# Kernel tuning notes

Measured on AMD Instinct MI355X. Metric: run time of the kernel, lower is better.

Reference implementation:

```python
import jax, jax.numpy as jnp
import numpy as np

N = 100000   # num nodes
E = 500000   # num hyperedges
NNZ = 1600000
H, C = 4, 32
IN_CH = 128


def setup_inputs() -> dict:
    key = jax.random.key(0)
    k1, k2, k3, k4, k5 = jax.random.split(key, 5)
    X = jax.random.normal(k1, (N, IN_CH), dtype=jnp.float32)
    W = jax.random.normal(k2, (IN_CH, H * C), dtype=jnp.float32) * (1.0 / np.sqrt(IN_CH))
    att_e = jax.random.normal(k3, (1, H, C), dtype=jnp.float32) * 0.1
    vertex = jax.random.randint(k4, (NNZ,), 0, N, dtype=jnp.int64)
    edges = jax.random.randint(k5, (NNZ,), 0, E, dtype=jnp.int64)
    return {"X": X, "W": W, "att_e": att_e, "vertex": vertex, "edges": edges}


def reference(X, W, att_e, vertex, edges):
    n = X.shape[0]
    X0 = X @ W                                  # [N, H*C]
    Xh = X0.reshape(n, H, C)                    # [N, H, C]
    Xve = Xh[vertex]                            # [nnz, H, C] gather
    # scatter-mean over hyperedges
    esum = jax.ops.segment_sum(Xve, edges, num_segments=E)            # [E, H, C]
    cnt = jax.ops.segment_sum(jnp.ones((Xve.shape[0],), X.dtype), edges, num_segments=E)
    Xe = esum / jnp.maximum(cnt, 1.0)[:, None, None]                  # [E, H, C]
    # per-edge attention score
    alpha_e = (Xe * att_e).sum(-1)              # [E, H]
    a_ev = alpha_e[edges]                       # [nnz, H]
    alpha = jax.nn.leaky_relu(a_ev, 0.01)
    # segment softmax over vertex groups
    m = jax.ops.segment_max(alpha, vertex, num_segments=n)            # [N, H]
    ex = jnp.exp(alpha - m[vertex])
    den = jax.ops.segment_sum(ex, vertex, num_segments=n)             # [N, H]
    alpha = ex / (den[vertex] + 1e-16)          # [nnz, H]
    # weighted scatter-sum back to nodes
    Xev = Xe[edges] * alpha[:, :, None]         # [nnz, H, C]
    Xv = jax.ops.segment_sum(Xev, vertex, num_segments=n)             # [N, H, C]
    return Xv.reshape(n, H * C) + X0
```

## Files before the change

### kernel.cpp

```cpp
#include <hip/hip_runtime.h>
#include <hip/hip_bf16.h>
#include <hip/hip_fp16.h>
#include <cstdint>

#define NH 4
#define HC 128
#define INCH 128
#define NEDGE 500000
#define NN 100000

#define KE_SHIFT 11
#define KV_SHIFT 9
#define KE (1 << KE_SHIFT)
#define KV (1 << KV_SHIFT)
#define NBE 245
#define NBV 196
#define CAP_E 8192
#define CAP_V 10240
#define CHUNK_A 8192
#define NB_ABS 64

typedef float          f32x2 __attribute__((ext_vector_type(2)));
typedef float          f32x4 __attribute__((ext_vector_type(4)));
typedef float          f32x8 __attribute__((ext_vector_type(8)));
typedef unsigned int   u32x2 __attribute__((ext_vector_type(2)));
typedef unsigned int   u32x4 __attribute__((ext_vector_type(4)));
typedef unsigned short u16x8 __attribute__((ext_vector_type(8)));

static __device__ __forceinline__ unsigned short f2bf(float f){
  union { float f; unsigned u; } v; v.f = f;
  unsigned r = v.u + 0x7fffu + ((v.u >> 16) & 1u);
  return (unsigned short)(r >> 16);
}
static __device__ __forceinline__ float bf2f(unsigned short b){
  union { unsigned u; float f; } v; v.u = ((unsigned)b) << 16;
  return v.f;
}
static __device__ __forceinline__ f32x8 bf8f(u16x8 b){
  f32x8 r;
  r[0]=bf2f(b[0]); r[1]=bf2f(b[1]); r[2]=bf2f(b[2]); r[3]=bf2f(b[3]);
  r[4]=bf2f(b[4]); r[5]=bf2f(b[5]); r[6]=bf2f(b[6]); r[7]=bf2f(b[7]);
  return r;
}

#if __has_builtin(__builtin_amdgcn_cvt_pk_fp8_f32) && __has_builtin(__builtin_amdgcn_cvt_pk_f32_fp8)
#define FP8_HW 1
#else
#define FP8_HW 0
#endif

#if !FP8_HW
static __device__ __forceinline__ unsigned enc1_fp8(float v){
  union{ __half h; unsigned short u; } c; c.h = __float2half(v);
  unsigned u = c.u;
  unsigned s = (u>>15)&1u, e=(u>>10)&31u, m=u&0x3FFu;
  int e8 = (int)e - 8;
  unsigned lsb = (m>>7)&1u;
  unsigned m8 = (m + 63u + lsb) >> 7;
  if (m8 == 8u){ m8 = 0u; e8 += 1; }
  if (e8 <= 0)  return s<<7;
  if (e8 >= 16) return (s<<7)|0x7Eu;
  return (s<<7)|((unsigned)e8<<3)|m8;
}
static __device__ __forceinline__ float dec1_fp8(unsigned b){
  unsigned s=(b>>7)&1u, e=(b>>3)&15u, m=b&7u;
  union{unsigned u; float f;} r;
  if (e==0u){ r.f = (float)m * 0.001953125f; if(s) r.f = -r.f; }
  else r.u = (s<<31)|((e+120u)<<23)|(m<<20);
  return r.f;
}
#endif

static __device__ __forceinline__ u32x2 pack8_fp8(const f32x8 v){
  u32x2 w;
#if FP8_HW
  int w0 = __builtin_amdgcn_cvt_pk_fp8_f32(v[0], v[1], 0, false);
  w0     = __builtin_amdgcn_cvt_pk_fp8_f32(v[2], v[3], w0, true);
  int w1 = __builtin_amdgcn_cvt_pk_fp8_f32(v[4], v[5], 0, false);
  w1     = __builtin_amdgcn_cvt_pk_fp8_f32(v[6], v[7], w1, true);
  w.x = (unsigned)w0; w.y = (unsigned)w1;
#else
  w.x = enc1_fp8(v[0]) | (enc1_fp8(v[1])<<8) | (enc1_fp8(v[2])<<16) | (enc1_fp8(v[3])<<24);
  w.y = enc1_fp8(v[4]) | (enc1_fp8(v[5])<<8) | (enc1_fp8(v[6])<<16) | (enc1_fp8(v[7])<<24);
#endif
  return w;
}
static __device__ __forceinline__ void fma8_fp8(f32x8& acc, float c, u32x2 q){
#if FP8_HW
  f32x2 p;
  p = __builtin_amdgcn_cvt_pk_f32_fp8((int)q.x, false); acc[0] += c*p.x; acc[1] += c*p.y;
  p = __builtin_amdgcn_cvt_pk_f32_fp8((int)q.x, true ); acc[2] += c*p.x; acc[3] += c*p.y;
  p = __builtin_amdgcn_cvt_pk_f32_fp8((int)q.y, false); acc[4] += c*p.x; acc[5] += c*p.y;
  p = __builtin_amdgcn_cvt_pk_f32_fp8((int)q.y, true ); acc[6] += c*p.x; acc[7] += c*p.y;
#else
  acc[0] += c*dec1_fp8(q.x&0xFF);        acc[1] += c*dec1_fp8((q.x>>8)&0xFF);
  acc[2] += c*dec1_fp8((q.x>>16)&0xFF);  acc[3] += c*dec1_fp8(q.x>>24);
  acc[4] += c*dec1_fp8(q.y&0xFF);        acc[5] += c*dec1_fp8((q.y>>8)&0xFF);
  acc[6] += c*dec1_fp8((q.y>>16)&0xFF);  acc[7] += c*dec1_fp8(q.y>>24);
#endif
}

#define GBM 128
#define GBK 16
__global__ __launch_bounds__(256, 2) void gemm_x0(const float* __restrict__ X,
                                                  const float* __restrict__ Wm,
                                                  unsigned short* __restrict__ X0bf, int nrows){
  __shared__ float As[GBK][GBM+4];
  __shared__ float Bs[GBK][HC+4];
  const int tid  = threadIdx.x;
  const int row0 = blockIdx.x * GBM;
  const int trow = tid >> 4;
  const int tcol = tid & 15;
  float acc[8][8];
  #pragma unroll
  for (int i=0;i<8;i++)
    #pragma unroll
    for (int j=0;j<8;j++) acc[i][j]=0.f;

  for (int k0=0;k0<INCH;k0+=GBK){
    #pragma unroll
    for (int l = tid; l < 512; l += 256){
      int r  = l >> 2;
      int ks = (l & 3) * 4;
      int grow = row0 + r;
      float4 v = make_float4(0.f,0.f,0.f,0.f);
      if (grow < nrows) v = *(const float4*)(X + (size_t)grow*INCH + k0 + ks);
      As[ks+0][r]=v.x; As[ks+1][r]=v.y; As[ks+2][r]=v.z; As[ks+3][r]=v.w;
    }
    #pragma unroll
    for (int l = tid; l < 512; l += 256){
      int r  = l >> 5;
      int cs = (l & 31) * 4;
      float4 v = *(const float4*)(Wm + (size_t)(k0+r)*HC + cs);
      *(float4*)(&Bs[r][cs]) = v;
    }
    __syncthreads();
    #pragma unroll
    for (int kk=0;kk<GBK;kk++){
      float a[8], b[8];
      *(float4*)&a[0] = *(float4*)&As[kk][trow*8];
      *(float4*)&a[4] = *(float4*)&As[kk][trow*8+4];
      *(float4*)&b[0] = *(float4*)&Bs[kk][tcol*8];
      *(float4*)&b[4] = *(float4*)&Bs[kk][tcol*8+4];
      #pragma unroll
      for (int i=0;i<8;i++)
        #pragma unroll
        for (int j=0;j<8;j++) acc[i][j] = fmaf(a[i], b[j], acc[i][j]);
    }
    __syncthreads();
  }
  #pragma unroll
  for (int i=0;i<8;i++){
    int grow = row0 + trow*8 + i;
    if (grow < nrows){
      ushort4 b0, b1;
      b0.x=f2bf(acc[i][0]); b0.y=f2bf(acc[i][1]); b0.z=f2bf(acc[i][2]); b0.w=f2bf(acc[i][3]);
      b1.x=f2bf(acc[i][4]); b1.y=f2bf(acc[i][5]); b1.z=f2bf(acc[i][6]); b1.w=f2bf(acc[i][7]);
      *(ushort4*)(X0bf + (size_t)grow*HC + tcol*8    ) = b0;
      *(ushort4*)(X0bf + (size_t)grow*HC + tcol*8 + 4) = b1;
    }
  }
}

__global__ __launch_bounds__(512) void phaseA(const unsigned short* __restrict__ X0bf,
                                              unsigned* __restrict__ gmaxU, int n8,
                                              const int* __restrict__ vertex,
                                              const int* __restrict__ edges, int nnz,
                                              int* __restrict__ cursE, int* __restrict__ cursV,
                                              unsigned* __restrict__ stgE, unsigned* __restrict__ stgV){
  __shared__ int cE[NBE], c2E[NBE], gE[NBE];
  __shared__ int cV[NBV], c2V[NBV], gV[NBV];
  __shared__ float red[8];
  const int t = threadIdx.x;

  if ((int)blockIdx.x < NB_ABS){
    float pm = 0.f;
    for (int i = blockIdx.x*512 + t; i < n8; i += NB_ABS*512){
      u16x8 v = *(const u16x8*)(X0bf + (size_t)i*8);
      f32x8 f = bf8f(v);
      #pragma unroll
      for (int j=0;j<8;j++) pm = fmaxf(pm, fabsf(f[j]));
    }
    #pragma unroll
    for (int s=1; s<64; s<<=1) pm = fmaxf(pm, __shfl_xor(pm, s, 64));
    const int wid = t >> 6;
    if ((t & 63) == 0) red[wid] = pm;
    __syncthreads();
    if (t == 0){
      float m = red[0];
      #pragma unroll
      for (int j=1;j<8;j++) m = fmaxf(m, red[j]);
      atomicMax(gmaxU, __float_as_uint(m));
    }
    return;
  }

  const int base = (blockIdx.x - NB_ABS) * CHUNK_A;
  int ev[16], vv[16];
  #pragma unroll
  for (int j=0;j<16;j++){
    int i = base + t + j*512;
    if (i < nnz){ ev[j] = edges[i]; vv[j] = vertex[i]; }
    else ev[j] = -1;
  }
  for (int j=t;j<NBE;j+=512){ cE[j]=0; c2E[j]=0; }
  for (int j=t;j<NBV;j+=512){ cV[j]=0; c2V[j]=0; }
  __syncthreads();
  #pragma unroll
  for (int j=0;j<16;j++) if (ev[j]>=0){
    atomicAdd(&cE[ev[j]>>KE_SHIFT], 1);
    atomicAdd(&cV[vv[j]>>KV_SHIFT], 1);
  }
  __syncthreads();
  for (int j=t;j<NBE;j+=512) gE[j] = atomicAdd(&cursE[j], cE[j]);
  for (int j=t;j<NBV;j+=512) gV[j] = atomicAdd(&cursV[j], cV[j]);
  __syncthreads();
  #pragma unroll
  for (int j=0;j<16;j++) if (ev[j]>=0){
    int bE = ev[j]>>KE_SHIFT;
    int p = gE[bE] + atomicAdd(&c2E[bE],1);
    if (p < CAP_E) stgE[(size_t)bE*CAP_E + p] = ((unsigned)vv[j] << KE_SHIFT) | (unsigned)(ev[j] & (KE-1));
    int bV = vv[j]>>KV_SHIFT;
    int q = gV[bV] + atomicAdd(&c2V[bV],1);
    if (q < CAP_V) stgV[(size_t)bV*CAP_V + q] = ((unsigned)ev[j] << KV_SHIFT) | (unsigned)(vv[j] & (KV-1));
  }
}

template<int K, int CAP, int IT, int SHIFT, int NB>
__device__ __forceinline__ void phaseB_body(const unsigned* __restrict__ stg,
                                            const int* __restrict__ curs,
                                            int* __restrict__ offsOut,
                                            int* __restrict__ csrOut, int nKeys, int b,
                                            int* cur, int* tsum, int* bsh){
  const int t = threadIdx.x;
  const int k0 = b * K;
  const int kc = min(K, nKeys - k0);
  int c = (t < NB) ? min(curs[t], CAP) : 0;
  bsh[t] = c; __syncthreads();
  for (int d2=1; d2<512; d2<<=1){
    int x = (t>=d2) ? bsh[t-d2] : 0; __syncthreads();
    bsh[t] += x; __syncthreads();
  }
  const int gbase = (b > 0) ? bsh[b-1] : 0;
  const int cnt   = min(curs[b], CAP);
  if (b == NB-1 && t == 0) offsOut[nKeys] = bsh[NB-1];
  unsigned it[IT];
  #pragma unroll
  for (int j=0;j<IT;j++){
    int i = t + j*512;
    it[j] = (i < cnt) ? stg[(size_t)b*CAP + i] : 0xFFFFFFFFu;
  }
  for (int j=t;j<K;j+=512) cur[j] = 0;
  __syncthreads();
  #pragma unroll
  for (int j=0;j<IT;j++) if (it[j] != 0xFFFFFFFFu) atomicAdd(&cur[it[j] & (K-1)], 1);
  __syncthreads();
  constexpr int KPT = K / 512;
  int loc[KPT]; int s = 0;
  #pragma unroll
  for (int j=0;j<KPT;j++){ loc[j] = s; s += cur[t*KPT + j]; }
  tsum[t] = s; __syncthreads();
  for (int d2=1; d2<512; d2<<=1){
    int x = (t>=d2) ? tsum[t-d2] : 0; __syncthreads();
    tsum[t] += x; __syncthreads();
  }
  const int tbase = tsum[t] - s;
  __syncthreads();
  #pragma unroll
  for (int j=0;j<KPT;j++){
    int k = t*KPT + j;
    int abs0 = gbase + tbase + loc[j];
    if (k < kc) offsOut[k0 + k] = abs0;
    cur[k] = abs0;
  }
  __syncthreads();
  #pragma unroll
  for (int j=0;j<IT;j++) if (it[j] != 0xFFFFFFFFu){
    int pos = atomicAdd(&cur[it[j] & (K-1)], 1);
    csrOut[pos] = (int)(it[j] >> SHIFT);
  }
}

__global__ __launch_bounds__(512) void phaseB_fused(const unsigned* __restrict__ stgE,
                                                    const unsigned* __restrict__ stgV,
                                                    const int* __restrict__ cursE,
                                                    const int* __restrict__ cursV,
                                                    int* __restrict__ eoffs, int* __restrict__ voffs,
                                                    int* __restrict__ ecsr, int* __restrict__ vcsr){
  __shared__ int cur[KE];
  __shared__ int tsum[512];
  __shared__ int bsh[512];
  const int b = blockIdx.x;
  if (b < NBE) phaseB_body<KE, CAP_E, CAP_E/512, KE_SHIFT, NBE>(stgE, cursE, eoffs, ecsr, NEDGE, b, cur, tsum, bsh);
  else         phaseB_body<KV, CAP_V, CAP_V/512, KV_SHIFT, NBV>(stgV, cursV, voffs, vcsr, NN, b - NBE, cur, tsum, bsh);
}

__global__ __launch_bounds__(256) void edge_agg(const unsigned short* __restrict__ X0bf,
                                                const float* __restrict__ att,
                                                const int* __restrict__ ecsr,
                                                const int* __restrict__ eoffs,
                                                const unsigned* __restrict__ gmaxU,
                                                unsigned char* __restrict__ Xe8,
                                                unsigned* __restrict__ alphaS, int E){
  int eg = blockIdx.x * 16 + (threadIdx.x >> 4);
  if (eg >= E) return;
  const int lane  = threadIdx.x & 15;
  const unsigned cbase = lane * 8;
  const float qs = 448.0f / fmaxf(__uint_as_float(*gmaxU), 1e-20f);
  float attv[8];
  *(f32x4*)&attv[0] = *(const f32x4*)(att + cbase);
  *(f32x4*)&attv[4] = *(const f32x4*)(att + cbase + 4);
  const int start = eoffs[eg];
  const int d     = eoffs[eg+1] - start;
  f32x8 acc0 = {0.f,0.f,0.f,0.f,0.f,0.f,0.f,0.f};
  f32x8 acc1 = {0.f,0.f,0.f,0.f,0.f,0.f,0.f,0.f};
  int k = 0;
  for (; k+1<d; k+=2){
    unsigned v0 = (unsigned)ecsr[start + k];
    unsigned v1 = (unsigned)ecsr[start + k + 1];
    u16x8 x0 = *(const u16x8*)(X0bf + v0*(unsigned)HC + cbase);
    u16x8 x1 = *(const u16x8*)(X0bf + v1*(unsigned)HC + cbase);
    acc0 += bf8f(x0);
    acc1 += bf8f(x1);
  }
  if (k < d){
    unsigned v0 = (unsigned)ecsr[start + k];
    u16x8 x0 = *(const u16x8*)(X0bf + v0*(unsigned)HC + cbase);
    acc0 += bf8f(x0);
  }
  acc0 += acc1;
  const float inv = 1.0f / fmaxf((float)d, 1.0f);
  acc0 *= inv;
  float p = 0.f;
  #pragma unroll
  for (int j=0;j<8;j++) p = fmaf(acc0[j], attv[j], p);
  p += __shfl_xor(p, 1, 4);
  p += __shfl_xor(p, 2, 4);
  float a = p > 0.f ? p : 0.01f*p;
  float e = __expf(a);
  f32x8 q = acc0 * qs;
  u32x2 w = pack8_fp8(q);
  *(u32x2*)(Xe8 + (unsigned)eg*(unsigned)HC + cbase) = w;
  float e0 = __shfl(e, 0, 16);
  float e1 = __shfl(e, 4, 16);
  float e2 = __shfl(e, 8, 16);
  float e3 = __shfl(e, 12, 16);
  if (lane == 0){
    u32x2 rec;
    rec.x = (unsigned)__half_as_ushort(__float2half(e0)) | ((unsigned)__half_as_ushort(__float2half(e1)) << 16);
    rec.y = (unsigned)__half_as_ushort(__float2half(e2)) | ((unsigned)__half_as_ushort(__float2half(e3)) << 16);
    *(u32x2*)(alphaS + (unsigned)eg*2u) = rec;
  }
}

__global__ __launch_bounds__(256) void vert_pass(const unsigned short* __restrict__ X0bf,
                                                 const unsigned char* __restrict__ Xe8,
                                                 const unsigned* __restrict__ alphaS,
                                                 const unsigned* __restrict__ gmaxU,
                                                 const int* __restrict__ vcsr,
                                                 const int* __restrict__ voffs,
                                                 float* __restrict__ out, int N){
  int n = blockIdx.x * 16 + (threadIdx.x >> 4);
  if (n >= N) return;
  const int lane  = threadIdx.x & 15;
  const unsigned cbase = lane * 8;
  const int h     = lane >> 2;
  const size_t obase = (size_t)n*HC + cbase;
  f32x8 x0 = bf8f(*(const u16x8*)(X0bf + obase));
  const int start = voffs[n];
  const int d     = voffs[n+1] - start;
  if (d == 0){
    f32x4 lo = {x0[0],x0[1],x0[2],x0[3]}, hi = {x0[4],x0[5],x0[6],x0[7]};
    __builtin_nontemporal_store(lo, (f32x4*)(out + obase));
    __builtin_nontemporal_store(hi, (f32x4*)(out + obase + 4));
    return;
  }
  const float dq = fmaxf(__uint_as_float(*gmaxU), 1e-20f) * (1.0f/448.0f);
  const u32x2 z2 = {0,0};

  float den0=0.f, den1=0.f, den2=0.f, den3=0.f;
  f32x8 acc0 = {0.f,0.f,0.f,0.f,0.f,0.f,0.f,0.f};
  f32x8 acc1 = {0.f,0.f,0.f,0.f,0.f,0.f,0.f,0.f};
  f32x8 acc2 = {0.f,0.f,0.f,0.f,0.f,0.f,0.f,0.f};
  f32x8 acc3 = {0.f,0.f,0.f,0.f,0.f,0.f,0.f,0.f};

#define UPD(i, rec, q) { \
    unsigned word_ = (h < 2) ? (rec).x : (rec).y; \
    unsigned h16_  = (h & 1) ? (word_ >> 16) : (word_ & 0xFFFFu); \
    float e_ = __half2float(__ushort_as_half((unsigned short)h16_)); \
    den##i += e_; \
    fma8_fp8(acc##i, e_, (q)); }

  for (int kb = 0; kb < d; kb += 16){
    int myidx = vcsr[start + min(kb + lane, d-1)];
    const int lim = min(16, d - kb);
    for (int j = 0; j < lim; j += 4){
      unsigned e0 = (unsigned)__shfl(myidx, j, 16);
      unsigned e1 = (unsigned)__shfl(myidx, min(j+1, 15), 16);
      unsigned e2 = (unsigned)__shfl(myidx, min(j+2, 15), 16);
      unsigned e3 = (unsigned)__shfl(myidx, min(j+3, 15), 16);
      u32x2 r0 = *(const u32x2*)(alphaS + e0*2u);
      u32x2 r1 = *(const u32x2*)(alphaS + e1*2u);
      u32x2 r2 = *(const u32x2*)(alphaS + e2*2u);
      u32x2 r3 = *(const u32x2*)(alphaS + e3*2u);
      u32x2 q0 = *(const u32x2*)(Xe8 + e0*(unsigned)HC + cbase);
      u32x2 q1 = *(const u32x2*)(Xe8 + e1*(unsigned)HC + cbase);
      u32x2 q2 = *(const u32x2*)(Xe8 + e2*(unsigned)HC + cbase);
      u32x2 q3 = *(const u32x2*)(Xe8 + e3*(unsigned)HC + cbase);
      r1 = (j+1 < lim) ? r1 : z2;
      r2 = (j+2 < lim) ? r2 : z2;
      r3 = (j+3 < lim) ? r3 : z2;
      UPD(0, r0, q0);
      UPD(1, r1, q1);
      UPD(2, r2, q2);
      UPD(3, r3, q3);
    }
  }
#undef UPD

  float den = (den0 + den1) + (den2 + den3);
  f32x8 acc = (acc0 + acc1) + (acc2 + acc3);
  const float w = dq / (den + 1e-16f);
  acc = acc*w + x0;
  f32x4 lo = {acc[0],acc[1],acc[2],acc[3]};
  f32x4 hi = {acc[4],acc[5],acc[6],acc[7]};
  __builtin_nontemporal_store(lo, (f32x4*)(out + obase));
  __builtin_nontemporal_store(hi, (f32x4*)(out + obase + 4));
}

extern "C" void kernel_launch(void* const* d_in, const int* in_sizes, int n_in,
                              void* d_out, int out_size, void* d_ws, size_t ws_size,
                              hipStream_t stream){
  const float* X   = (const float*)d_in[0];
  const float* Wm  = (const float*)d_in[1];
  const float* att = (const float*)d_in[2];
  const int* vertex = (const int*)d_in[3];
  const int* edges  = (const int*)d_in[4];
  const int N   = in_sizes[0] / INCH;
  const int NNZ = in_sizes[3];
  const int E   = NEDGE;

  char* ws = (char*)d_ws;
  size_t off = 0;
  auto alloc = [&](size_t bytes)->char*{
    char* p = ws + off;
    off += (bytes + 255) & ~(size_t)255;
    return p;
  };
  unsigned char*  Xe8    = (unsigned char*)alloc((size_t)E * HC);
  unsigned short* X0bf   = (unsigned short*)alloc((size_t)NN * HC * sizeof(unsigned short));
  unsigned*       alphaS = (unsigned*)alloc((size_t)E * 2 * sizeof(unsigned));
  int*            eoffs  = (int*)alloc((size_t)(E+1) * sizeof(int));
  int*            voffs  = (int*)alloc((size_t)(NN+1) * sizeof(int));
  int*            ecsr   = (int*)alloc((size_t)NNZ * sizeof(int));
  int*            vcsr   = (int*)alloc((size_t)NNZ * sizeof(int));
  int*            curs   = (int*)alloc((size_t)(NBE + NBV + 1) * sizeof(int));
  int*            cursE  = curs;
  int*            cursV  = curs + NBE;
  unsigned*       gmaxU  = (unsigned*)(curs + NBE + NBV);
  unsigned* stgE = (unsigned*)(void*)Xe8;
  unsigned* stgV = (unsigned*)((char*)(void*)Xe8 + (size_t)NBE * CAP_E * sizeof(unsigned));

  const int nA = (NNZ + CHUNK_A - 1) / CHUNK_A;

  hipMemsetAsync(curs, 0, (size_t)(NBE + NBV + 1) * sizeof(int), stream);
  gemm_x0<<<(N + GBM - 1)/GBM, 256, 0, stream>>>(X, Wm, X0bf, N);
  phaseA<<<NB_ABS + nA, 512, 0, stream>>>(X0bf, gmaxU, N * HC / 8,
                                          vertex, edges, NNZ, cursE, cursV, stgE, stgV);
  phaseB_fused<<<NBE + NBV, 512, 0, stream>>>(stgE, stgV, cursE, cursV, eoffs, voffs, ecsr, vcsr);
  edge_agg<<<(E + 15)/16, 256, 0, stream>>>(X0bf, att, ecsr, eoffs, gmaxU, Xe8, alphaS, E);
  vert_pass<<<(N + 15)/16, 256, 0, stream>>>(X0bf, Xe8, alphaS, gmaxU, vcsr, voffs, (float*)d_out, N);
}
```

Measured before the change: 249.5 us.

## Sort edges and vertices by degree buckets to balance aggregation waves

Builds a per-degree histogram during CSR construction, scans it, and scatters packed (start, degree, id) records into degree-sorted order. The edge and vertex aggregation kernels then iterate over these sorted records so groups in a wavefront have similar loop trip counts. This targets divergence from uneven segment sizes, at the cost of two extra small kernels, extra record traffic, and less sequential locality in output writes. Degrees are clamped to 2047 in the packed record.

```diff
diff --git a/kernel.cpp b/kernel.cpp
--- a/kernel.cpp
+++ b/kernel.cpp
@@ -19,6 +19,8 @@
 #define CAP_V 10240
 #define CHUNK_A 8192
 #define NB_ABS 64
+#define NBIN 64
+#define NB_SORT 128
 
 typedef float          f32x2 __attribute__((ext_vector_type(2)));
 typedef float          f32x4 __attribute__((ext_vector_type(4)));
@@ -100,6 +102,12 @@
 #endif
 }
 
+static __device__ __forceinline__ unsigned long long packRec(int start, int d, int id){
+  return (unsigned long long)(unsigned)start
+       | ((unsigned long long)(unsigned)min(d, 2047) << 21)
+       | ((unsigned long long)(unsigned)id << 32);
+}
+
 #define GBM 128
 #define GBK 16
 __global__ __launch_bounds__(256, 2) void gemm_x0(const float* __restrict__ X,
@@ -231,7 +239,8 @@
                                             const int* __restrict__ curs,
                                             int* __restrict__ offsOut,
                                             int* __restrict__ csrOut, int nKeys, int b,
-                                            int* cur, int* tsum, int* bsh){
+                                            int* cur, int* tsum, int* bsh,
+                                            int* dh, int* __restrict__ dhist){
   const int t = threadIdx.x;
   const int k0 = b * K;
   const int kc = min(K, nKeys - k0);
@@ -251,6 +260,7 @@
     it[j] = (i < cnt) ? stg[(size_t)b*CAP + i] : 0xFFFFFFFFu;
   }
   for (int j=t;j<K;j+=512) cur[j] = 0;
+  if (t < NBIN) dh[t] = 0;
   __syncthreads();
   #pragma unroll
   for (int j=0;j<IT;j++) if (it[j] != 0xFFFFFFFFu) atomicAdd(&cur[it[j] & (K-1)], 1);
@@ -258,7 +268,11 @@
   constexpr int KPT = K / 512;
   int loc[KPT]; int s = 0;
   #pragma unroll
-  for (int j=0;j<KPT;j++){ loc[j] = s; s += cur[t*KPT + j]; }
+  for (int j=0;j<KPT;j++){
+    int c_ = cur[t*KPT + j];
+    loc[j] = s; s += c_;
+    if (t*KPT + j < kc) atomicAdd(&dh[min(c_, NBIN-1)], 1);
+  }
   tsum[t] = s; __syncthreads();
   for (int d2=1; d2<512; d2<<=1){
     int x = (t>=d2) ? tsum[t-d2] : 0; __syncthreads();
@@ -266,6 +280,7 @@
   }
   const int tbase = tsum[t] - s;
   __syncthreads();
+  if (t < NBIN) atomicAdd(&dhist[t], dh[t]);
   #pragma unroll
   for (int j=0;j<KPT;j++){
     int k = t*KPT + j;
@@ -286,32 +301,81 @@
                                                     const int* __restrict__ cursE,
                                                     const int* __restrict__ cursV,
                                                     int* __restrict__ eoffs, int* __restrict__ voffs,
-                                                    int* __restrict__ ecsr, int* __restrict__ vcsr){
+                                                    int* __restrict__ ecsr, int* __restrict__ vcsr,
+                                                    int* __restrict__ dhistE, int* __restrict__ dhistV){
   __shared__ int cur[KE];
   __shared__ int tsum[512];
   __shared__ int bsh[512];
+  __shared__ int dh[NBIN];
   const int b = blockIdx.x;
-  if (b < NBE) phaseB_body<KE, CAP_E, CAP_E/512, KE_SHIFT, NBE>(stgE, cursE, eoffs, ecsr, NEDGE, b, cur, tsum, bsh);
-  else         phaseB_body<KV, CAP_V, CAP_V/512, KV_SHIFT, NBV>(stgV, cursV, voffs, vcsr, NN, b - NBE, cur, tsum, bsh);
+  if (b < NBE) phaseB_body<KE, CAP_E, CAP_E/512, KE_SHIFT, NBE>(stgE, cursE, eoffs, ecsr, NEDGE, b, cur, tsum, bsh, dh, dhistE);
+  else         phaseB_body<KV, CAP_V, CAP_V/512, KV_SHIFT, NBV>(stgV, cursV, voffs, vcsr, NN, b - NBE, cur, tsum, bsh, dh, dhistV);
+}
+
+__global__ __launch_bounds__(64) void dscan(const int* __restrict__ dhistE, const int* __restrict__ dhistV,
+                                            int* __restrict__ fillE, int* __restrict__ fillV){
+  if (threadIdx.x == 0){
+    int s = 0;
+    for (int i=0;i<NBIN;i++){ fillE[i] = s; s += dhistE[i]; }
+  } else if (threadIdx.x == 1){
+    int s = 0;
+    for (int i=0;i<NBIN;i++){ fillV[i] = s; s += dhistV[i]; }
+  }
+}
+
+__global__ __launch_bounds__(512) void dscat(const int* __restrict__ eoffs, const int* __restrict__ voffs,
+                                             int* __restrict__ fillE, int* __restrict__ fillV,
+                                             unsigned long long* __restrict__ eRec,
+                                             unsigned long long* __restrict__ vRec){
+  __shared__ int cnt[NBIN], gb[NBIN], curb[NBIN];
+  const int t = threadIdx.x;
+  const bool isE = (int)blockIdx.x < NB_SORT;
+  const int rb   = isE ? (int)blockIdx.x : (int)blockIdx.x - NB_SORT;
+  const int nKeys = isE ? NEDGE : NN;
+  const int chunk = (nKeys + NB_SORT - 1) / NB_SORT;
+  const int k0 = rb * chunk;
+  const int kend = min(k0 + chunk, nKeys);
+  const int* offs = isE ? eoffs : voffs;
+  int* fill = isE ? fillE : fillV;
+  unsigned long long* rec = isE ? eRec : vRec;
+
+  if (t < NBIN){ cnt[t] = 0; curb[t] = 0; }
+  __syncthreads();
+  for (int k = k0 + t; k < kend; k += 512){
+    int d = offs[k+1] - offs[k];
+    atomicAdd(&cnt[min(d, NBIN-1)], 1);
+  }
+  __syncthreads();
+  if (t < NBIN) gb[t] = atomicAdd(&fill[t], cnt[t]);
+  __syncthreads();
+  for (int k = k0 + t; k < kend; k += 512){
+    int st = offs[k];
+    int d  = offs[k+1] - st;
+    int bin = min(d, NBIN-1);
+    int pos = gb[bin] + atomicAdd(&curb[bin], 1);
+    rec[pos] = packRec(st, d, k);
+  }
 }
 
 __global__ __launch_bounds__(256) void edge_agg(const unsigned short* __restrict__ X0bf,
                                                 const float* __restrict__ att,
                                                 const int* __restrict__ ecsr,
-                                                const int* __restrict__ eoffs,
+                                                const unsigned long long* __restrict__ eRec,
                                                 const unsigned* __restrict__ gmaxU,
                                                 unsigned char* __restrict__ Xe8,
                                                 unsigned* __restrict__ alphaS, int E){
-  int eg = blockIdx.x * 16 + (threadIdx.x >> 4);
-  if (eg >= E) return;
+  int gid = blockIdx.x * 16 + (threadIdx.x >> 4);
+  if (gid >= E) return;
   const int lane  = threadIdx.x & 15;
   const unsigned cbase = lane * 8;
   const float qs = 448.0f / fmaxf(__uint_as_float(*gmaxU), 1e-20f);
   float attv[8];
   *(f32x4*)&attv[0] = *(const f32x4*)(att + cbase);
   *(f32x4*)&attv[4] = *(const f32x4*)(att + cbase + 4);
-  const int start = eoffs[eg];
-  const int d     = eoffs[eg+1] - start;
+  const unsigned long long rc = eRec[gid];
+  const int start = (int)(rc & 0x1FFFFFu);
+  const int d     = (int)((rc >> 21) & 0x7FFu);
+  const int eg    = (int)(rc >> 32);
   f32x8 acc0 = {0.f,0.f,0.f,0.f,0.f,0.f,0.f,0.f};
   f32x8 acc1 = {0.f,0.f,0.f,0.f,0.f,0.f,0.f,0.f};
   int k = 0;
@@ -358,17 +422,19 @@
                                                  const unsigned* __restrict__ alphaS,
                                                  const unsigned* __restrict__ gmaxU,
                                                  const int* __restrict__ vcsr,
-                                                 const int* __restrict__ voffs,
+                                                 const unsigned long long* __restrict__ vRec,
                                                  float* __restrict__ out, int N){
-  int n = blockIdx.x * 16 + (threadIdx.x >> 4);
-  if (n >= N) return;
+  int gid = blockIdx.x * 16 + (threadIdx.x >> 4);
+  if (gid >= N) return;
   const int lane  = threadIdx.x & 15;
   const unsigned cbase = lane * 8;
   const int h     = lane >> 2;
+  const unsigned long long rc = vRec[gid];
+  const int start = (int)(rc & 0x1FFFFFu);
+  const int d     = (int)((rc >> 21) & 0x7FFu);
+  const int n     = (int)(rc >> 32);
   const size_t obase = (size_t)n*HC + cbase;
   f32x8 x0 = bf8f(*(const u16x8*)(X0bf + obase));
-  const int start = voffs[n];
-  const int d     = voffs[n+1] - start;
   if (d == 0){
     f32x4 lo = {x0[0],x0[1],x0[2],x0[3]}, hi = {x0[4],x0[5],x0[6],x0[7]};
     __builtin_nontemporal_store(lo, (f32x4*)(out + obase));
@@ -454,20 +520,29 @@
   int*            voffs  = (int*)alloc((size_t)(NN+1) * sizeof(int));
   int*            ecsr   = (int*)alloc((size_t)NNZ * sizeof(int));
   int*            vcsr   = (int*)alloc((size_t)NNZ * sizeof(int));
-  int*            curs   = (int*)alloc((size_t)(NBE + NBV + 1) * sizeof(int));
+  unsigned long long* eRec = (unsigned long long*)alloc((size_t)E * 8);
+  unsigned long long* vRec = (unsigned long long*)alloc((size_t)NN * 8);
+  int*            curs   = (int*)alloc((size_t)(NBE + NBV + 1 + 4*NBIN) * sizeof(int));
   int*            cursE  = curs;
   int*            cursV  = curs + NBE;
   unsigned*       gmaxU  = (unsigned*)(curs + NBE + NBV);
+  int*            dhistE = curs + NBE + NBV + 1;
+  int*            dhistV = dhistE + NBIN;
+  int*            fillE  = dhistV + NBIN;
+  int*            fillV  = fillE + NBIN;
   unsigned* stgE = (unsigned*)(void*)Xe8;
   unsigned* stgV = (unsigned*)((char*)(void*)Xe8 + (size_t)NBE * CAP_E * sizeof(unsigned));
 
   const int nA = (NNZ + CHUNK_A - 1) / CHUNK_A;
 
-  hipMemsetAsync(curs, 0, (size_t)(NBE + NBV + 1) * sizeof(int), stream);
+  hipMemsetAsync(curs, 0, (size_t)(NBE + NBV + 1 + 4*NBIN) * sizeof(int), stream);
   gemm_x0<<<(N + GBM - 1)/GBM, 256, 0, stream>>>(X, Wm, X0bf, N);
   phaseA<<<NB_ABS + nA, 512, 0, stream>>>(X0bf, gmaxU, N * HC / 8,
                                           vertex, edges, NNZ, cursE, cursV, stgE, stgV);
-  phaseB_fused<<<NBE + NBV, 512, 0, stream>>>(stgE, stgV, cursE, cursV, eoffs, voffs, ecsr, vcsr);
-  edge_agg<<<(E + 15)/16, 256, 0, stream>>>(X0bf, att, ecsr, eoffs, gmaxU, Xe8, alphaS, E);
-  vert_pass<<<(N + 15)/16, 256, 0, stream>>>(X0bf, Xe8, alphaS, gmaxU, vcsr, voffs, (float*)d_out, N);
-}
+  phaseB_fused<<<NBE + NBV, 512, 0, stream>>>(stgE, stgV, cursE, cursV, eoffs, voffs, ecsr, vcsr,
+                                              dhistE, dhistV);
+  dscan<<<1, 64, 0, stream>>>(dhistE, dhistV, fillE, fillV);
+  dscat<<<2*NB_SORT, 512, 0, stream>>>(eoffs, voffs, fillE, fillV, eRec, vRec);
+  edge_agg<<<(E + 15)/16, 256, 0, stream>>>(X0bf, att, ecsr, eRec, gmaxU, Xe8, alphaS, E);
+  vert_pass<<<(N + 15)/16, 256, 0, stream>>>(X0bf, Xe8, alphaS, gmaxU, vcsr, vRec, (float*)d_out, N);
+}
```

Result: slower. 268.7 us (+7.7%).
